# Performance work log

Measured on AMD Instinct MI355X. Metric: run time of the kernel, lower is better.

The kernel has to match this reference:

```python
import jax, jax.numpy as jnp
import numpy as np

B, S, H, D = 2, 4096, 16, 64


def setup_inputs() -> dict:
    key = jax.random.key(0)
    qkv = jax.random.normal(key, (B, S, 3, H, D), dtype=jnp.float32)
    return {"qkv": qkv}


def reference(qkv) -> jnp.ndarray:
    batch, seq_len, three, num_heads, head_dim = qkv.shape
    softmax_scale = head_dim ** (-0.5)
    q = qkv[:, :, 0]  # (B, S, H, D)
    k = qkv[:, :, 1]
    v = qkv[:, :, 2]
    # (B, H, S, S) score matrix, faithful to the naive matmul+mask+softmax path
    scores = jnp.einsum('bshd,bthd->bhst', q, k) * softmax_scale
    row = jnp.arange(seq_len)[:, None]
    col = jnp.arange(seq_len)[None, :]
    causal = row >= col  # (S, S) bool
    scores = jnp.where(causal[None, None, :, :], scores, -1000000000.0)
    attn = jax.nn.softmax(scores, axis=-1)
    out = jnp.einsum('bhst,bthd->bshd', attn, v)  # (B, S, H, D)
    return out
```

## Files before the change

kernel.cpp:

```cpp
#include <hip/hip_runtime.h>


#define S_LEN 4096
#define NHEAD 16
#define HDIM 64
#define QBLK 128
#define KVBLK 64
#define NQT (S_LEN / QBLK)
#define LDK 72
#define ROWSTRIDE (3 * NHEAD * HDIM)

using bf16x8 = __attribute__((ext_vector_type(8))) short;
using bf16x4 = __attribute__((ext_vector_type(4))) short;
using f32x4  = __attribute__((ext_vector_type(4))) float;

#define MFMA32(A, B, C) __builtin_amdgcn_mfma_f32_16x16x32_bf16((A), (B), (C), 0, 0, 0)
#define MFMA16(A, B, C) __builtin_amdgcn_mfma_f32_16x16x16bf16_1k((A), (B), (C), 0, 0, 0)

#if __has_builtin(__builtin_amdgcn_exp2f)
#define EXP2F(x) __builtin_amdgcn_exp2f(x)
#else
#define EXP2F(x) exp2f(x)
#endif

__device__ __forceinline__ int f2bf2(float lo, float hi) {
  int r;
  asm("v_cvt_pk_bf16_f32 %0, %1, %2" : "=v"(r) : "v"(lo), "v"(hi));
  return r;
}

__device__ __forceinline__ float max3f(float a, float b, float c) {
  float d;
  asm("v_max3_f32 %0, %1, %2, %3" : "=v"(d) : "v"(a), "v"(b), "v"(c));
  return d;
}

__global__ __launch_bounds__(256, 2)
void attn_fwd(const float* __restrict__ qkv, float* __restrict__ out) {
  __shared__ short Ks[KVBLK][LDK] __attribute__((aligned(16)));
  __shared__ short VTs[HDIM][LDK] __attribute__((aligned(16)));

  const int flat = (int)blockIdx.x + 32 * (int)blockIdx.y;
  const int u    = flat & 255;
  const int j    = flat >> 8;
  const int bh   = u >> 3;
  const int t8   = u & 7;
  const int qt   = (j == 0) ? t8 : (j == 1) ? 31 - t8 : (j == 2) ? 8 + t8 : 23 - t8;

  const int b    = bh >> 4;
  const int h    = bh & 15;
  const int tid  = threadIdx.x;
  const int wid  = tid >> 6;
  const int lane = tid & 63;
  const int lq   = lane & 15;
  const int lg   = lane >> 4;

  const float* basep = qkv + (size_t)b * S_LEN * ROWSTRIDE + h * HDIM;
  const float* kbase = basep + NHEAD * HDIM;
  const float* vbase = basep + 2 * NHEAD * HDIM;

  const int rb = (tid >> 4) * 4;
  const int cb = (tid & 15) * 4;
  const int vcol = 4 * ((rb >> 2) ^ (cb >> 3));

  f32x4 kreg[4], vreg[4];
  auto load_tile = [&](int kvt) {
    const int kr = kvt * KVBLK + rb;
#pragma unroll
    for (int i = 0; i < 4; ++i) {
      kreg[i] = *reinterpret_cast<const f32x4*>(kbase + (size_t)(kr + i) * ROWSTRIDE + cb);
      vreg[i] = *reinterpret_cast<const f32x4*>(vbase + (size_t)(kr + i) * ROWSTRIDE + cb);
    }
  };
  auto store_tile = [&]() {
#pragma unroll
    for (int i = 0; i < 4; ++i) {
      union { bf16x4 v; int w[2]; } kk;
      kk.w[0] = f2bf2(kreg[i][0], kreg[i][1]);
      kk.w[1] = f2bf2(kreg[i][2], kreg[i][3]);
      *reinterpret_cast<bf16x4*>(&Ks[rb + i][cb]) = kk.v;
    }
#pragma unroll
    for (int e = 0; e < 4; ++e) {
      union { bf16x4 v; int w[2]; } vv;
      vv.w[0] = f2bf2(vreg[0][e], vreg[1][e]);
      vv.w[1] = f2bf2(vreg[2][e], vreg[3][e]);
      *reinterpret_cast<bf16x4*>(&VTs[cb + e][vcol]) = vv.v;
    }
  };

  const float SC = 0.18033688011112042f;

  const int wq = qt * QBLK + wid * 32;

  bf16x8 qf[2][2];
#pragma unroll
  for (int rt = 0; rt < 2; ++rt) {
    const float* qp = basep + (size_t)(wq + rt * 16 + lq) * ROWSTRIDE + 8 * lg;
#pragma unroll
    for (int t = 0; t < 2; ++t) {
      f32x4 x0 = *reinterpret_cast<const f32x4*>(qp + 32 * t);
      f32x4 x1 = *reinterpret_cast<const f32x4*>(qp + 32 * t + 4);
      union { bf16x8 v; int w[4]; } uq;
      uq.w[0] = f2bf2(x0[0] * SC, x0[1] * SC);
      uq.w[1] = f2bf2(x0[2] * SC, x0[3] * SC);
      uq.w[2] = f2bf2(x1[0] * SC, x1[1] * SC);
      uq.w[3] = f2bf2(x1[2] * SC, x1[3] * SC);
      qf[rt][t] = uq.v;
    }
  }

  f32x4 acc[2][4];
#pragma unroll
  for (int rt = 0; rt < 2; ++rt)
#pragma unroll
    for (int dt = 0; dt < 4; ++dt)
      acc[rt][dt] = (f32x4){0.f, 0.f, 0.f, 0.f};

  float mrun[2] = {-1e30f, -1e30f};
  float lrun[2] = {0.f, 0.f};

  const int nkv = 2 * qt + 2;
  load_tile(0);

  for (int kvt = 0; kvt < nkv; ++kvt) {
    __syncthreads();
    store_tile();
    __syncthreads();
    if (kvt + 1 < nkv) load_tile(kvt + 1);

    const int kvb = kvt * KVBLK;
    if (kvb > wq + 31) continue;

    f32x4 sc[2][4];
#pragma unroll
    for (int rt = 0; rt < 2; ++rt)
#pragma unroll
      for (int c = 0; c < 4; ++c)
        sc[rt][c] = (f32x4){0.f, 0.f, 0.f, 0.f};

#pragma unroll
    for (int c = 0; c < 4; ++c) {
      bf16x8 k0 = *reinterpret_cast<const bf16x8*>(&Ks[c * 16 + lq][8 * lg]);
      bf16x8 k1 = *reinterpret_cast<const bf16x8*>(&Ks[c * 16 + lq][8 * lg + 32]);
#pragma unroll
      for (int rt = 0; rt < 2; ++rt) {
        sc[rt][c] = MFMA32(k0, qf[rt][0], sc[rt][c]);
        sc[rt][c] = MFMA32(k1, qf[rt][1], sc[rt][c]);
      }
    }

    if (kvb + KVBLK - 1 > wq) {
#pragma unroll
      for (int rt = 0; rt < 2; ++rt) {
        const int q0 = wq + rt * 16 + lq;
#pragma unroll
        for (int c = 0; c < 4; ++c)
#pragma unroll
          for (int r = 0; r < 4; ++r)
            if (kvb + c * 16 + 4 * lg + r > q0) sc[rt][c][r] = -1e30f;
      }
    }

    bf16x4 pf[2][4];
    float alpha[2];
#pragma unroll
    for (int rt = 0; rt < 2; ++rt) {
      float v0 = max3f(sc[rt][0][0], sc[rt][0][1], sc[rt][0][2]);
      float v1 = max3f(sc[rt][0][3], sc[rt][1][0], sc[rt][1][1]);
      float v2 = max3f(sc[rt][1][2], sc[rt][1][3], sc[rt][2][0]);
      float v3 = max3f(sc[rt][2][1], sc[rt][2][2], sc[rt][2][3]);
      float v4 = max3f(sc[rt][3][0], sc[rt][3][1], sc[rt][3][2]);
      float tm = fmaxf(max3f(v0, v1, v2), max3f(v3, v4, sc[rt][3][3]));
      tm = fmaxf(tm, __shfl_xor(tm, 16));
      tm = fmaxf(tm, __shfl_xor(tm, 32));
      const float newm = fmaxf(mrun[rt], tm);
      alpha[rt] = EXP2F(mrun[rt] - newm);
      mrun[rt] = newm;

      float ts = 0.f;
#pragma unroll
      for (int c = 0; c < 4; ++c) {
        float p0 = EXP2F(sc[rt][c][0] - newm);
        float p1 = EXP2F(sc[rt][c][1] - newm);
        float p2 = EXP2F(sc[rt][c][2] - newm);
        float p3 = EXP2F(sc[rt][c][3] - newm);
        ts += (p0 + p1) + (p2 + p3);
        union { bf16x4 v; int w[2]; } pp;
        pp.w[0] = f2bf2(p0, p1);
        pp.w[1] = f2bf2(p2, p3);
        pf[rt][c] = pp.v;
      }
      ts += __shfl_xor(ts, 16);
      ts += __shfl_xor(ts, 32);
      lrun[rt] = lrun[rt] * alpha[rt] + ts;
    }

#pragma unroll
    for (int rt = 0; rt < 2; ++rt) {
      const float a0 = __shfl(alpha[rt], 4 * lg + 0);
      const float a1 = __shfl(alpha[rt], 4 * lg + 1);
      const float a2 = __shfl(alpha[rt], 4 * lg + 2);
      const float a3 = __shfl(alpha[rt], 4 * lg + 3);
#pragma unroll
      for (int dt = 0; dt < 4; ++dt) {
        acc[rt][dt][0] *= a0;
        acc[rt][dt][1] *= a1;
        acc[rt][dt][2] *= a2;
        acc[rt][dt][3] *= a3;
      }
    }

#pragma unroll
    for (int dt = 0; dt < 4; ++dt) {
      const int f = (2 * dt + (lq >> 3)) & 7;
#pragma unroll
      for (int c = 0; c < 4; ++c) {
        bf16x4 vf = *reinterpret_cast<const bf16x4*>(&VTs[dt * 16 + lq][4 * ((4 * c + lg) ^ f)]);
        acc[0][dt] = MFMA16(pf[0][c], vf, acc[0][dt]);
        acc[1][dt] = MFMA16(pf[1][c], vf, acc[1][dt]);
      }
    }
  }

#pragma unroll
  for (int rt = 0; rt < 2; ++rt) {
    const float l0 = __shfl(lrun[rt], 4 * lg + 0);
    const float l1 = __shfl(lrun[rt], 4 * lg + 1);
    const float l2 = __shfl(lrun[rt], 4 * lg + 2);
    const float l3 = __shfl(lrun[rt], 4 * lg + 3);
    const f32x4 linv = {1.f / l0, 1.f / l1, 1.f / l2, 1.f / l3};
#pragma unroll
    for (int dt = 0; dt < 4; ++dt) {
#pragma unroll
      for (int r = 0; r < 4; ++r) {
        out[(size_t)(b * S_LEN + wq + rt * 16 + 4 * lg + r) * (NHEAD * HDIM) + h * HDIM + dt * 16 + lq] =
            acc[rt][dt][r] * linv[r];
      }
    }
  }
}

extern "C" void kernel_launch(void* const* d_in, const int* in_sizes, int n_in,
                              void* d_out, int out_size, void* d_ws, size_t ws_size,
                              hipStream_t stream) {
  const float* qkv = (const float*)d_in[0];
  float* o = (float*)d_out;
  dim3 grid(NQT, 2 * NHEAD);
  attn_fwd<<<grid, 256, 0, stream>>>(qkv, o);
}
```

Measured before the change: 182.4 us.

## Use 256-row Q blocks with 8 waves and paired causal tiles per block

The Q block grows to 256 rows with 512 threads (8 waves), so each K/V tile staged in LDS serves twice as many query rows. Each block now handles two query tiles, qt and 15-qt, one after the other, which evens out causal work across blocks. Staging is split so half the threads load and convert K and the other half load V. The risk is that 512 blocks of 512 threads may fill the 256 CUs less well than before, and that waves which skip fully masked tiles sit idle at the barriers.

```diff
diff --git a/kernel.cpp b/kernel.cpp
--- a/kernel.cpp
+++ b/kernel.cpp
@@ -4,9 +4,9 @@
 #define S_LEN 4096
 #define NHEAD 16
 #define HDIM 64
-#define QBLK 128
+#define QBLK 256
 #define KVBLK 64
-#define NQT (S_LEN / QBLK)
+#define NPAIR 16
 #define LDK 72
 #define ROWSTRIDE (3 * NHEAD * HDIM)
 
@@ -35,18 +35,13 @@
   return d;
 }
 
-__global__ __launch_bounds__(256, 2)
+__global__ __launch_bounds__(512, 2)
 void attn_fwd(const float* __restrict__ qkv, float* __restrict__ out) {
   __shared__ short Ks[KVBLK][LDK] __attribute__((aligned(16)));
   __shared__ short VTs[HDIM][LDK] __attribute__((aligned(16)));
 
-  const int flat = (int)blockIdx.x + 32 * (int)blockIdx.y;
-  const int u    = flat & 255;
-  const int j    = flat >> 8;
-  const int bh   = u >> 3;
-  const int t8   = u & 7;
-  const int qt   = (j == 0) ? t8 : (j == 1) ? 31 - t8 : (j == 2) ? 8 + t8 : 23 - t8;
-
+  const int qp0  = blockIdx.x;
+  const int bh   = blockIdx.y;
   const int b    = bh >> 4;
   const int h    = bh & 15;
   const int tid  = threadIdx.x;
@@ -59,183 +54,200 @@
   const float* kbase = basep + NHEAD * HDIM;
   const float* vbase = basep + 2 * NHEAD * HDIM;
 
-  const int rb = (tid >> 4) * 4;
-  const int cb = (tid & 15) * 4;
-  const int vcol = 4 * ((rb >> 2) ^ (cb >> 3));
-
-  f32x4 kreg[4], vreg[4];
+  const bool isK = tid < 256;
+  const int st   = tid & 255;
+  const int krow = st >> 2;
+  const int kcol = (st & 3) * 16;
+  const int vrb  = (st >> 4) * 4;
+  const int vcb  = (st & 15) * 4;
+  const int vcol = 4 * ((vrb >> 2) ^ (vcb >> 3));
+
+  f32x4 sreg[4];
   auto load_tile = [&](int kvt) {
-    const int kr = kvt * KVBLK + rb;
-#pragma unroll
-    for (int i = 0; i < 4; ++i) {
-      kreg[i] = *reinterpret_cast<const f32x4*>(kbase + (size_t)(kr + i) * ROWSTRIDE + cb);
-      vreg[i] = *reinterpret_cast<const f32x4*>(vbase + (size_t)(kr + i) * ROWSTRIDE + cb);
+    if (isK) {
+      const float* p = kbase + (size_t)(kvt * KVBLK + krow) * ROWSTRIDE + kcol;
+      sreg[0] = *reinterpret_cast<const f32x4*>(p);
+      sreg[1] = *reinterpret_cast<const f32x4*>(p + 4);
+      sreg[2] = *reinterpret_cast<const f32x4*>(p + 8);
+      sreg[3] = *reinterpret_cast<const f32x4*>(p + 12);
+    } else {
+      const float* p = vbase + (size_t)(kvt * KVBLK + vrb) * ROWSTRIDE + vcb;
+#pragma unroll
+      for (int i = 0; i < 4; ++i)
+        sreg[i] = *reinterpret_cast<const f32x4*>(p + (size_t)i * ROWSTRIDE);
     }
   };
   auto store_tile = [&]() {
-#pragma unroll
-    for (int i = 0; i < 4; ++i) {
-      union { bf16x4 v; int w[2]; } kk;
-      kk.w[0] = f2bf2(kreg[i][0], kreg[i][1]);
-      kk.w[1] = f2bf2(kreg[i][2], kreg[i][3]);
-      *reinterpret_cast<bf16x4*>(&Ks[rb + i][cb]) = kk.v;
-    }
-#pragma unroll
-    for (int e = 0; e < 4; ++e) {
-      union { bf16x4 v; int w[2]; } vv;
-      vv.w[0] = f2bf2(vreg[0][e], vreg[1][e]);
-      vv.w[1] = f2bf2(vreg[2][e], vreg[3][e]);
-      *reinterpret_cast<bf16x4*>(&VTs[cb + e][vcol]) = vv.v;
+    if (isK) {
+      union { bf16x8 v; int w[4]; } u0, u1;
+      u0.w[0] = f2bf2(sreg[0][0], sreg[0][1]); u0.w[1] = f2bf2(sreg[0][2], sreg[0][3]);
+      u0.w[2] = f2bf2(sreg[1][0], sreg[1][1]); u0.w[3] = f2bf2(sreg[1][2], sreg[1][3]);
+      u1.w[0] = f2bf2(sreg[2][0], sreg[2][1]); u1.w[1] = f2bf2(sreg[2][2], sreg[2][3]);
+      u1.w[2] = f2bf2(sreg[3][0], sreg[3][1]); u1.w[3] = f2bf2(sreg[3][2], sreg[3][3]);
+      *reinterpret_cast<bf16x8*>(&Ks[krow][kcol])     = u0.v;
+      *reinterpret_cast<bf16x8*>(&Ks[krow][kcol + 8]) = u1.v;
+    } else {
+#pragma unroll
+      for (int e = 0; e < 4; ++e) {
+        union { bf16x4 v; int w[2]; } vv;
+        vv.w[0] = f2bf2(sreg[0][e], sreg[1][e]);
+        vv.w[1] = f2bf2(sreg[2][e], sreg[3][e]);
+        *reinterpret_cast<bf16x4*>(&VTs[vcb + e][vcol]) = vv.v;
+      }
     }
   };
 
   const float SC = 0.18033688011112042f;
 
-  const int wq = qt * QBLK + wid * 32;
-
-  bf16x8 qf[2][2];
-#pragma unroll
-  for (int rt = 0; rt < 2; ++rt) {
-    const float* qp = basep + (size_t)(wq + rt * 16 + lq) * ROWSTRIDE + 8 * lg;
-#pragma unroll
-    for (int t = 0; t < 2; ++t) {
-      f32x4 x0 = *reinterpret_cast<const f32x4*>(qp + 32 * t);
-      f32x4 x1 = *reinterpret_cast<const f32x4*>(qp + 32 * t + 4);
-      union { bf16x8 v; int w[4]; } uq;
-      uq.w[0] = f2bf2(x0[0] * SC, x0[1] * SC);
-      uq.w[1] = f2bf2(x0[2] * SC, x0[3] * SC);
-      uq.w[2] = f2bf2(x1[0] * SC, x1[1] * SC);
-      uq.w[3] = f2bf2(x1[2] * SC, x1[3] * SC);
-      qf[rt][t] = uq.v;
-    }
-  }
-
-  f32x4 acc[2][4];
-#pragma unroll
-  for (int rt = 0; rt < 2; ++rt)
-#pragma unroll
-    for (int dt = 0; dt < 4; ++dt)
-      acc[rt][dt] = (f32x4){0.f, 0.f, 0.f, 0.f};
-
-  float mrun[2] = {-1e30f, -1e30f};
-  float lrun[2] = {0.f, 0.f};
-
-  const int nkv = 2 * qt + 2;
-  load_tile(0);
-
-  for (int kvt = 0; kvt < nkv; ++kvt) {
-    __syncthreads();
-    store_tile();
-    __syncthreads();
-    if (kvt + 1 < nkv) load_tile(kvt + 1);
-
-    const int kvb = kvt * KVBLK;
-    if (kvb > wq + 31) continue;
-
-    f32x4 sc[2][4];
+#pragma unroll 1
+  for (int pi = 0; pi < 2; ++pi) {
+    const int qt = (pi == 0) ? qp0 : (NPAIR - 1 - qp0);
+    const int wq = qt * QBLK + wid * 32;
+
+    bf16x8 qf[2][2];
+#pragma unroll
+    for (int rt = 0; rt < 2; ++rt) {
+      const float* qp = basep + (size_t)(wq + rt * 16 + lq) * ROWSTRIDE + 8 * lg;
+#pragma unroll
+      for (int t = 0; t < 2; ++t) {
+        f32x4 x0 = *reinterpret_cast<const f32x4*>(qp + 32 * t);
+        f32x4 x1 = *reinterpret_cast<const f32x4*>(qp + 32 * t + 4);
+        union { bf16x8 v; int w[4]; } uq;
+        uq.w[0] = f2bf2(x0[0] * SC, x0[1] * SC);
+        uq.w[1] = f2bf2(x0[2] * SC, x0[3] * SC);
+        uq.w[2] = f2bf2(x1[0] * SC, x1[1] * SC);
+        uq.w[3] = f2bf2(x1[2] * SC, x1[3] * SC);
+        qf[rt][t] = uq.v;
+      }
+    }
+
+    f32x4 acc[2][4];
 #pragma unroll
     for (int rt = 0; rt < 2; ++rt)
 #pragma unroll
-      for (int c = 0; c < 4; ++c)
-        sc[rt][c] = (f32x4){0.f, 0.f, 0.f, 0.f};
-
-#pragma unroll
-    for (int c = 0; c < 4; ++c) {
-      bf16x8 k0 = *reinterpret_cast<const bf16x8*>(&Ks[c * 16 + lq][8 * lg]);
-      bf16x8 k1 = *reinterpret_cast<const bf16x8*>(&Ks[c * 16 + lq][8 * lg + 32]);
+      for (int dt = 0; dt < 4; ++dt)
+        acc[rt][dt] = (f32x4){0.f, 0.f, 0.f, 0.f};
+
+    float mrun[2] = {-1e30f, -1e30f};
+    float lrun[2] = {0.f, 0.f};
+
+    const int nkv = 4 * qt + 4;
+    load_tile(0);
+
+    for (int kvt = 0; kvt < nkv; ++kvt) {
+      __syncthreads();
+      store_tile();
+      __syncthreads();
+      if (kvt + 1 < nkv) load_tile(kvt + 1);
+
+      const int kvb = kvt * KVBLK;
+      if (kvb > wq + 31) continue;
+
+      f32x4 sc[2][4];
+#pragma unroll
+      for (int rt = 0; rt < 2; ++rt)
+#pragma unroll
+        for (int c = 0; c < 4; ++c)
+          sc[rt][c] = (f32x4){0.f, 0.f, 0.f, 0.f};
+
+#pragma unroll
+      for (int c = 0; c < 4; ++c) {
+        bf16x8 k0 = *reinterpret_cast<const bf16x8*>(&Ks[c * 16 + lq][8 * lg]);
+        bf16x8 k1 = *reinterpret_cast<const bf16x8*>(&Ks[c * 16 + lq][8 * lg + 32]);
+#pragma unroll
+        for (int rt = 0; rt < 2; ++rt) {
+          sc[rt][c] = MFMA32(k0, qf[rt][0], sc[rt][c]);
+          sc[rt][c] = MFMA32(k1, qf[rt][1], sc[rt][c]);
+        }
+      }
+
+      if (kvb + KVBLK - 1 > wq) {
+#pragma unroll
+        for (int rt = 0; rt < 2; ++rt) {
+          const int q0 = wq + rt * 16 + lq;
+#pragma unroll
+          for (int c = 0; c < 4; ++c)
+#pragma unroll
+            for (int r = 0; r < 4; ++r)
+              if (kvb + c * 16 + 4 * lg + r > q0) sc[rt][c][r] = -1e30f;
+        }
+      }
+
+      bf16x4 pf[2][4];
+      float alpha[2];
 #pragma unroll
       for (int rt = 0; rt < 2; ++rt) {
-        sc[rt][c] = MFMA32(k0, qf[rt][0], sc[rt][c]);
-        sc[rt][c] = MFMA32(k1, qf[rt][1], sc[rt][c]);
-      }
-    }
-
-    if (kvb + KVBLK - 1 > wq) {
+        float v0 = max3f(sc[rt][0][0], sc[rt][0][1], sc[rt][0][2]);
+        float v1 = max3f(sc[rt][0][3], sc[rt][1][0], sc[rt][1][1]);
+        float v2 = max3f(sc[rt][1][2], sc[rt][1][3], sc[rt][2][0]);
+        float v3 = max3f(sc[rt][2][1], sc[rt][2][2], sc[rt][2][3]);
+        float v4 = max3f(sc[rt][3][0], sc[rt][3][1], sc[rt][3][2]);
+        float tm = fmaxf(max3f(v0, v1, v2), max3f(v3, v4, sc[rt][3][3]));
+        tm = fmaxf(tm, __shfl_xor(tm, 16));
+        tm = fmaxf(tm, __shfl_xor(tm, 32));
+        const float newm = fmaxf(mrun[rt], tm);
+        alpha[rt] = EXP2F(mrun[rt] - newm);
+        mrun[rt] = newm;
+
+        float ts = 0.f;
+#pragma unroll
+        for (int c = 0; c < 4; ++c) {
+          float p0 = EXP2F(sc[rt][c][0] - newm);
+          float p1 = EXP2F(sc[rt][c][1] - newm);
+          float p2 = EXP2F(sc[rt][c][2] - newm);
+          float p3 = EXP2F(sc[rt][c][3] - newm);
+          ts += (p0 + p1) + (p2 + p3);
+          union { bf16x4 v; int w[2]; } pp;
+          pp.w[0] = f2bf2(p0, p1);
+          pp.w[1] = f2bf2(p2, p3);
+          pf[rt][c] = pp.v;
+        }
+        ts += __shfl_xor(ts, 16);
+        ts += __shfl_xor(ts, 32);
+        lrun[rt] = lrun[rt] * alpha[rt] + ts;
+      }
+
 #pragma unroll
       for (int rt = 0; rt < 2; ++rt) {
-        const int q0 = wq + rt * 16 + lq;
-#pragma unroll
-        for (int c = 0; c < 4; ++c)
-#pragma unroll
-          for (int r = 0; r < 4; ++r)
-            if (kvb + c * 16 + 4 * lg + r > q0) sc[rt][c][r] = -1e30f;
-      }
-    }
-
-    bf16x4 pf[2][4];
-    float alpha[2];
+        const float a0 = __shfl(alpha[rt], 4 * lg + 0);
+        const float a1 = __shfl(alpha[rt], 4 * lg + 1);
+        const float a2 = __shfl(alpha[rt], 4 * lg + 2);
+        const float a3 = __shfl(alpha[rt], 4 * lg + 3);
+#pragma unroll
+        for (int dt = 0; dt < 4; ++dt) {
+          acc[rt][dt][0] *= a0;
+          acc[rt][dt][1] *= a1;
+          acc[rt][dt][2] *= a2;
+          acc[rt][dt][3] *= a3;
+        }
+      }
+
+#pragma unroll
+      for (int dt = 0; dt < 4; ++dt) {
+        const int f = (2 * dt + (lq >> 3)) & 7;
+#pragma unroll
+        for (int c = 0; c < 4; ++c) {
+          bf16x4 vf = *reinterpret_cast<const bf16x4*>(&VTs[dt * 16 + lq][4 * ((4 * c + lg) ^ f)]);
+          acc[0][dt] = MFMA16(pf[0][c], vf, acc[0][dt]);
+          acc[1][dt] = MFMA16(pf[1][c], vf, acc[1][dt]);
+        }
+      }
+    }
+
 #pragma unroll
     for (int rt = 0; rt < 2; ++rt) {
-      float v0 = max3f(sc[rt][0][0], sc[rt][0][1], sc[rt][0][2]);
-      float v1 = max3f(sc[rt][0][3], sc[rt][1][0], sc[rt][1][1]);
-      float v2 = max3f(sc[rt][1][2], sc[rt][1][3], sc[rt][2][0]);
-      float v3 = max3f(sc[rt][2][1], sc[rt][2][2], sc[rt][2][3]);
-      float v4 = max3f(sc[rt][3][0], sc[rt][3][1], sc[rt][3][2]);
-      float tm = fmaxf(max3f(v0, v1, v2), max3f(v3, v4, sc[rt][3][3]));
-      tm = fmaxf(tm, __shfl_xor(tm, 16));
-      tm = fmaxf(tm, __shfl_xor(tm, 32));
-      const float newm = fmaxf(mrun[rt], tm);
-      alpha[rt] = EXP2F(mrun[rt] - newm);
-      mrun[rt] = newm;
-
-      float ts = 0.f;
-#pragma unroll
-      for (int c = 0; c < 4; ++c) {
-        float p0 = EXP2F(sc[rt][c][0] - newm);
-        float p1 = EXP2F(sc[rt][c][1] - newm);
-        float p2 = EXP2F(sc[rt][c][2] - newm);
-        float p3 = EXP2F(sc[rt][c][3] - newm);
-        ts += (p0 + p1) + (p2 + p3);
-        union { bf16x4 v; int w[2]; } pp;
-        pp.w[0] = f2bf2(p0, p1);
-        pp.w[1] = f2bf2(p2, p3);
-        pf[rt][c] = pp.v;
-      }
-      ts += __shfl_xor(ts, 16);
-      ts += __shfl_xor(ts, 32);
-      lrun[rt] = lrun[rt] * alpha[rt] + ts;
-    }
-
-#pragma unroll
-    for (int rt = 0; rt < 2; ++rt) {
-      const float a0 = __shfl(alpha[rt], 4 * lg + 0);
-      const float a1 = __shfl(alpha[rt], 4 * lg + 1);
-      const float a2 = __shfl(alpha[rt], 4 * lg + 2);
-      const float a3 = __shfl(alpha[rt], 4 * lg + 3);
+      const float l0 = __shfl(lrun[rt], 4 * lg + 0);
+      const float l1 = __shfl(lrun[rt], 4 * lg + 1);
+      const float l2 = __shfl(lrun[rt], 4 * lg + 2);
+      const float l3 = __shfl(lrun[rt], 4 * lg + 3);
+      const f32x4 linv = {1.f / l0, 1.f / l1, 1.f / l2, 1.f / l3};
 #pragma unroll
       for (int dt = 0; dt < 4; ++dt) {
-        acc[rt][dt][0] *= a0;
-        acc[rt][dt][1] *= a1;
-        acc[rt][dt][2] *= a2;
-        acc[rt][dt][3] *= a3;
-      }
-    }
-
-#pragma unroll
-    for (int dt = 0; dt < 4; ++dt) {
-      const int f = (2 * dt + (lq >> 3)) & 7;
-#pragma unroll
-      for (int c = 0; c < 4; ++c) {
-        bf16x4 vf = *reinterpret_cast<const bf16x4*>(&VTs[dt * 16 + lq][4 * ((4 * c + lg) ^ f)]);
-        acc[0][dt] = MFMA16(pf[0][c], vf, acc[0][dt]);
-        acc[1][dt] = MFMA16(pf[1][c], vf, acc[1][dt]);
-      }
-    }
-  }
-
-#pragma unroll
-  for (int rt = 0; rt < 2; ++rt) {
-    const float l0 = __shfl(lrun[rt], 4 * lg + 0);
-    const float l1 = __shfl(lrun[rt], 4 * lg + 1);
-    const float l2 = __shfl(lrun[rt], 4 * lg + 2);
-    const float l3 = __shfl(lrun[rt], 4 * lg + 3);
-    const f32x4 linv = {1.f / l0, 1.f / l1, 1.f / l2, 1.f / l3};
-#pragma unroll
-    for (int dt = 0; dt < 4; ++dt) {
-#pragma unroll
-      for (int r = 0; r < 4; ++r) {
-        out[(size_t)(b * S_LEN + wq + rt * 16 + 4 * lg + r) * (NHEAD * HDIM) + h * HDIM + dt * 16 + lq] =
-            acc[rt][dt][r] * linv[r];
+#pragma unroll
+        for (int r = 0; r < 4; ++r) {
+          out[(size_t)(b * S_LEN + wq + rt * 16 + 4 * lg + r) * (NHEAD * HDIM) + h * HDIM + dt * 16 + lq] =
+              acc[rt][dt][r] * linv[r];
+        }
       }
     }
   }
@@ -246,6 +258,6 @@
                               hipStream_t stream) {
   const float* qkv = (const float*)d_in[0];
   float* o = (float*)d_out;
-  dim3 grid(NQT, 2 * NHEAD);
-  attn_fwd<<<grid, 256, 0, stream>>>(qkv, o);
-}
+  dim3 grid(NPAIR, 2 * NHEAD);
+  attn_fwd<<<grid, 512, 0, stream>>>(qkv, o);
+}
```

Measured after the change: 262.2 us. 43.8% more time.

## Precompute bf16 K and transposed V into workspace, read directly from global

Applied to the files above, without the earlier changes.

Adds a pre-pass kernel that converts K to bf16 and writes V transposed in bf16 into the workspace buffer. The attention kernel then loads its MFMA fragments straight from global or L2, with no LDS staging and no __syncthreads. Each wave also stops at its own causal bound instead of looping over the whole block's tile count. This removes repeated fp32 conversion, the barriers, and LDS traffic, at the cost of an extra launch and uncoalesced small global loads that are not double-buffered. The old path is kept as a fallback for when the workspace is too small.

```diff
diff --git a/kernel.cpp b/kernel.cpp
--- a/kernel.cpp
+++ b/kernel.cpp
@@ -9,6 +9,7 @@
 #define NQT (S_LEN / QBLK)
 #define LDK 72
 #define ROWSTRIDE (3 * NHEAD * HDIM)
+#define KB_ELEMS ((size_t)2 * NHEAD * S_LEN * HDIM)
 
 using bf16x8 = __attribute__((ext_vector_type(8))) short;
 using bf16x4 = __attribute__((ext_vector_type(4))) short;
@@ -36,10 +37,56 @@
 }
 
 __global__ __launch_bounds__(256, 2)
-void attn_fwd(const float* __restrict__ qkv, float* __restrict__ out) {
-  __shared__ short Ks[KVBLK][LDK] __attribute__((aligned(16)));
-  __shared__ short VTs[HDIM][LDK] __attribute__((aligned(16)));
-
+void precompute_kv(const float* __restrict__ qkv, short* __restrict__ Kb,
+                   short* __restrict__ VTb) {
+  const int s0 = blockIdx.x * 64;
+  const int bh = blockIdx.y;
+  const int b  = bh >> 4;
+  const int h  = bh & 15;
+  const int tid = threadIdx.x;
+  const float* basep = qkv + (size_t)b * S_LEN * ROWSTRIDE + h * HDIM;
+  const float* kbase = basep + NHEAD * HDIM;
+  const float* vbase = basep + 2 * NHEAD * HDIM;
+
+  {
+    const int krow = tid >> 2;
+    const int kcol = (tid & 3) * 16;
+    const float* p = kbase + (size_t)(s0 + krow) * ROWSTRIDE + kcol;
+    f32x4 a0 = *reinterpret_cast<const f32x4*>(p);
+    f32x4 a1 = *reinterpret_cast<const f32x4*>(p + 4);
+    f32x4 a2 = *reinterpret_cast<const f32x4*>(p + 8);
+    f32x4 a3 = *reinterpret_cast<const f32x4*>(p + 12);
+    union { bf16x8 v; int w[4]; } u0, u1;
+    u0.w[0] = f2bf2(a0[0], a0[1]); u0.w[1] = f2bf2(a0[2], a0[3]);
+    u0.w[2] = f2bf2(a1[0], a1[1]); u0.w[3] = f2bf2(a1[2], a1[3]);
+    u1.w[0] = f2bf2(a2[0], a2[1]); u1.w[1] = f2bf2(a2[2], a2[3]);
+    u1.w[2] = f2bf2(a3[0], a3[1]); u1.w[3] = f2bf2(a3[2], a3[3]);
+    short* dst = Kb + ((size_t)bh * S_LEN + s0 + krow) * HDIM + kcol;
+    *reinterpret_cast<bf16x8*>(dst)     = u0.v;
+    *reinterpret_cast<bf16x8*>(dst + 8) = u1.v;
+  }
+  {
+    const int vrb = (tid >> 4) * 4;
+    const int vcb = (tid & 15) * 4;
+    const float* p = vbase + (size_t)(s0 + vrb) * ROWSTRIDE + vcb;
+    f32x4 r0 = *reinterpret_cast<const f32x4*>(p);
+    f32x4 r1 = *reinterpret_cast<const f32x4*>(p + ROWSTRIDE);
+    f32x4 r2 = *reinterpret_cast<const f32x4*>(p + 2 * ROWSTRIDE);
+    f32x4 r3 = *reinterpret_cast<const f32x4*>(p + 3 * ROWSTRIDE);
+#pragma unroll
+    for (int e = 0; e < 4; ++e) {
+      union { bf16x4 v; int w[2]; } vv;
+      vv.w[0] = f2bf2(r0[e], r1[e]);
+      vv.w[1] = f2bf2(r2[e], r3[e]);
+      short* dst = VTb + ((size_t)bh * HDIM + vcb + e) * S_LEN + s0 + vrb;
+      *reinterpret_cast<bf16x4*>(dst) = vv.v;
+    }
+  }
+}
+
+__global__ __launch_bounds__(256, 2)
+void attn_fwd(const float* __restrict__ qkv, const short* __restrict__ Kb,
+              const short* __restrict__ VTb, float* __restrict__ out) {
   const int flat = (int)blockIdx.x + 32 * (int)blockIdx.y;
   const int u    = flat & 255;
   const int j    = flat >> 8;
@@ -56,39 +103,6 @@
   const int lg   = lane >> 4;
 
   const float* basep = qkv + (size_t)b * S_LEN * ROWSTRIDE + h * HDIM;
-  const float* kbase = basep + NHEAD * HDIM;
-  const float* vbase = basep + 2 * NHEAD * HDIM;
-
-  const int rb = (tid >> 4) * 4;
-  const int cb = (tid & 15) * 4;
-  const int vcol = 4 * ((rb >> 2) ^ (cb >> 3));
-
-  f32x4 kreg[4], vreg[4];
-  auto load_tile = [&](int kvt) {
-    const int kr = kvt * KVBLK + rb;
-#pragma unroll
-    for (int i = 0; i < 4; ++i) {
-      kreg[i] = *reinterpret_cast<const f32x4*>(kbase + (size_t)(kr + i) * ROWSTRIDE + cb);
-      vreg[i] = *reinterpret_cast<const f32x4*>(vbase + (size_t)(kr + i) * ROWSTRIDE + cb);
-    }
-  };
-  auto store_tile = [&]() {
-#pragma unroll
-    for (int i = 0; i < 4; ++i) {
-      union { bf16x4 v; int w[2]; } kk;
-      kk.w[0] = f2bf2(kreg[i][0], kreg[i][1]);
-      kk.w[1] = f2bf2(kreg[i][2], kreg[i][3]);
-      *reinterpret_cast<bf16x4*>(&Ks[rb + i][cb]) = kk.v;
-    }
-#pragma unroll
-    for (int e = 0; e < 4; ++e) {
-      union { bf16x4 v; int w[2]; } vv;
-      vv.w[0] = f2bf2(vreg[0][e], vreg[1][e]);
-      vv.w[1] = f2bf2(vreg[2][e], vreg[3][e]);
-      *reinterpret_cast<bf16x4*>(&VTs[cb + e][vcol]) = vv.v;
-    }
-  };
-
   const float SC = 0.18033688011112042f;
 
   const int wq = qt * QBLK + wid * 32;
@@ -120,17 +134,14 @@
   float mrun[2] = {-1e30f, -1e30f};
   float lrun[2] = {0.f, 0.f};
 
-  const int nkv = 2 * qt + 2;
-  load_tile(0);
-
+  const int nkv = ((wq + 31) >> 6) + 1;
+
+  const short* kwave = Kb + ((size_t)bh * S_LEN + lq) * HDIM + 8 * lg;
+  const short* vwave = VTb + ((size_t)bh * HDIM + lq) * S_LEN + 4 * lg;
+
+#pragma unroll 1
   for (int kvt = 0; kvt < nkv; ++kvt) {
-    __syncthreads();
-    store_tile();
-    __syncthreads();
-    if (kvt + 1 < nkv) load_tile(kvt + 1);
-
     const int kvb = kvt * KVBLK;
-    if (kvb > wq + 31) continue;
 
     f32x4 sc[2][4];
 #pragma unroll
@@ -141,8 +152,9 @@
 
 #pragma unroll
     for (int c = 0; c < 4; ++c) {
-      bf16x8 k0 = *reinterpret_cast<const bf16x8*>(&Ks[c * 16 + lq][8 * lg]);
-      bf16x8 k1 = *reinterpret_cast<const bf16x8*>(&Ks[c * 16 + lq][8 * lg + 32]);
+      const short* kp = kwave + (size_t)(kvb + c * 16) * HDIM;
+      bf16x8 k0 = *reinterpret_cast<const bf16x8*>(kp);
+      bf16x8 k1 = *reinterpret_cast<const bf16x8*>(kp + 32);
 #pragma unroll
       for (int rt = 0; rt < 2; ++rt) {
         sc[rt][c] = MFMA32(k0, qf[rt][0], sc[rt][c]);
@@ -213,10 +225,10 @@
 
 #pragma unroll
     for (int dt = 0; dt < 4; ++dt) {
-      const int f = (2 * dt + (lq >> 3)) & 7;
+      const short* vp = vwave + (size_t)(dt * 16) * S_LEN + kvb;
 #pragma unroll
       for (int c = 0; c < 4; ++c) {
-        bf16x4 vf = *reinterpret_cast<const bf16x4*>(&VTs[dt * 16 + lq][4 * ((4 * c + lg) ^ f)]);
+        bf16x4 vf = *reinterpret_cast<const bf16x4*>(vp + c * 16);
         acc[0][dt] = MFMA16(pf[0][c], vf, acc[0][dt]);
         acc[1][dt] = MFMA16(pf[1][c], vf, acc[1][dt]);
       }
@@ -241,11 +253,222 @@
   }
 }
 
+__global__ __launch_bounds__(256, 2)
+void attn_fwd_fb(const float* __restrict__ qkv, float* __restrict__ out) {
+  __shared__ short Ks[KVBLK][LDK] __attribute__((aligned(16)));
+  __shared__ short VTs[HDIM][LDK] __attribute__((aligned(16)));
+
+  const int flat = (int)blockIdx.x + 32 * (int)blockIdx.y;
+  const int u    = flat & 255;
+  const int j    = flat >> 8;
+  const int bh   = u >> 3;
+  const int t8   = u & 7;
+  const int qt   = (j == 0) ? t8 : (j == 1) ? 31 - t8 : (j == 2) ? 8 + t8 : 23 - t8;
+
+  const int b    = bh >> 4;
+  const int h    = bh & 15;
+  const int tid  = threadIdx.x;
+  const int wid  = tid >> 6;
+  const int lane = tid & 63;
+  const int lq   = lane & 15;
+  const int lg   = lane >> 4;
+
+  const float* basep = qkv + (size_t)b * S_LEN * ROWSTRIDE + h * HDIM;
+  const float* kbase = basep + NHEAD * HDIM;
+  const float* vbase = basep + 2 * NHEAD * HDIM;
+
+  const int rb = (tid >> 4) * 4;
+  const int cb = (tid & 15) * 4;
+  const int vcol = 4 * ((rb >> 2) ^ (cb >> 3));
+
+  f32x4 kreg[4], vreg[4];
+  auto load_tile = [&](int kvt) {
+    const int kr = kvt * KVBLK + rb;
+#pragma unroll
+    for (int i = 0; i < 4; ++i) {
+      kreg[i] = *reinterpret_cast<const f32x4*>(kbase + (size_t)(kr + i) * ROWSTRIDE + cb);
+      vreg[i] = *reinterpret_cast<const f32x4*>(vbase + (size_t)(kr + i) * ROWSTRIDE + cb);
+    }
+  };
+  auto store_tile = [&]() {
+#pragma unroll
+    for (int i = 0; i < 4; ++i) {
+      union { bf16x4 v; int w[2]; } kk;
+      kk.w[0] = f2bf2(kreg[i][0], kreg[i][1]);
+      kk.w[1] = f2bf2(kreg[i][2], kreg[i][3]);
+      *reinterpret_cast<bf16x4*>(&Ks[rb + i][cb]) = kk.v;
+    }
+#pragma unroll
+    for (int e = 0; e < 4; ++e) {
+      union { bf16x4 v; int w[2]; } vv;
+      vv.w[0] = f2bf2(vreg[0][e], vreg[1][e]);
+      vv.w[1] = f2bf2(vreg[2][e], vreg[3][e]);
+      *reinterpret_cast<bf16x4*>(&VTs[cb + e][vcol]) = vv.v;
+    }
+  };
+
+  const float SC = 0.18033688011112042f;
+  const int wq = qt * QBLK + wid * 32;
+
+  bf16x8 qf[2][2];
+#pragma unroll
+  for (int rt = 0; rt < 2; ++rt) {
+    const float* qp = basep + (size_t)(wq + rt * 16 + lq) * ROWSTRIDE + 8 * lg;
+#pragma unroll
+    for (int t = 0; t < 2; ++t) {
+      f32x4 x0 = *reinterpret_cast<const f32x4*>(qp + 32 * t);
+      f32x4 x1 = *reinterpret_cast<const f32x4*>(qp + 32 * t + 4);
+      union { bf16x8 v; int w[4]; } uq;
+      uq.w[0] = f2bf2(x0[0] * SC, x0[1] * SC);
+      uq.w[1] = f2bf2(x0[2] * SC, x0[3] * SC);
+      uq.w[2] = f2bf2(x1[0] * SC, x1[1] * SC);
+      uq.w[3] = f2bf2(x1[2] * SC, x1[3] * SC);
+      qf[rt][t] = uq.v;
+    }
+  }
+
+  f32x4 acc[2][4];
+#pragma unroll
+  for (int rt = 0; rt < 2; ++rt)
+#pragma unroll
+    for (int dt = 0; dt < 4; ++dt)
+      acc[rt][dt] = (f32x4){0.f, 0.f, 0.f, 0.f};
+
+  float mrun[2] = {-1e30f, -1e30f};
+  float lrun[2] = {0.f, 0.f};
+
+  const int nkv = 2 * qt + 2;
+  load_tile(0);
+
+  for (int kvt = 0; kvt < nkv; ++kvt) {
+    __syncthreads();
+    store_tile();
+    __syncthreads();
+    if (kvt + 1 < nkv) load_tile(kvt + 1);
+
+    const int kvb = kvt * KVBLK;
+    if (kvb > wq + 31) continue;
+
+    f32x4 sc[2][4];
+#pragma unroll
+    for (int rt = 0; rt < 2; ++rt)
+#pragma unroll
+      for (int c = 0; c < 4; ++c)
+        sc[rt][c] = (f32x4){0.f, 0.f, 0.f, 0.f};
+
+#pragma unroll
+    for (int c = 0; c < 4; ++c) {
+      bf16x8 k0 = *reinterpret_cast<const bf16x8*>(&Ks[c * 16 + lq][8 * lg]);
+      bf16x8 k1 = *reinterpret_cast<const bf16x8*>(&Ks[c * 16 + lq][8 * lg + 32]);
+#pragma unroll
+      for (int rt = 0; rt < 2; ++rt) {
+        sc[rt][c] = MFMA32(k0, qf[rt][0], sc[rt][c]);
+        sc[rt][c] = MFMA32(k1, qf[rt][1], sc[rt][c]);
+      }
+    }
+
+    if (kvb + KVBLK - 1 > wq) {
+#pragma unroll
+      for (int rt = 0; rt < 2; ++rt) {
+        const int q0 = wq + rt * 16 + lq;
+#pragma unroll
+        for (int c = 0; c < 4; ++c)
+#pragma unroll
+          for (int r = 0; r < 4; ++r)
+            if (kvb + c * 16 + 4 * lg + r > q0) sc[rt][c][r] = -1e30f;
+      }
+    }
+
+    bf16x4 pf[2][4];
+    float alpha[2];
+#pragma unroll
+    for (int rt = 0; rt < 2; ++rt) {
+      float v0 = max3f(sc[rt][0][0], sc[rt][0][1], sc[rt][0][2]);
+      float v1 = max3f(sc[rt][0][3], sc[rt][1][0], sc[rt][1][1]);
+      float v2 = max3f(sc[rt][1][2], sc[rt][1][3], sc[rt][2][0]);
+      float v3 = max3f(sc[rt][2][1], sc[rt][2][2], sc[rt][2][3]);
+      float v4 = max3f(sc[rt][3][0], sc[rt][3][1], sc[rt][3][2]);
+      float tm = fmaxf(max3f(v0, v1, v2), max3f(v3, v4, sc[rt][3][3]));
+      tm = fmaxf(tm, __shfl_xor(tm, 16));
+      tm = fmaxf(tm, __shfl_xor(tm, 32));
+      const float newm = fmaxf(mrun[rt], tm);
+      alpha[rt] = EXP2F(mrun[rt] - newm);
+      mrun[rt] = newm;
+
+      float ts = 0.f;
+#pragma unroll
+      for (int c = 0; c < 4; ++c) {
+        float p0 = EXP2F(sc[rt][c][0] - newm);
+        float p1 = EXP2F(sc[rt][c][1] - newm);
+        float p2 = EXP2F(sc[rt][c][2] - newm);
+        float p3 = EXP2F(sc[rt][c][3] - newm);
+        ts += (p0 + p1) + (p2 + p3);
+        union { bf16x4 v; int w[2]; } pp;
+        pp.w[0] = f2bf2(p0, p1);
+        pp.w[1] = f2bf2(p2, p3);
+        pf[rt][c] = pp.v;
+      }
+      ts += __shfl_xor(ts, 16);
+      ts += __shfl_xor(ts, 32);
+      lrun[rt] = lrun[rt] * alpha[rt] + ts;
+    }
+
+#pragma unroll
+    for (int rt = 0; rt < 2; ++rt) {
+      const float a0 = __shfl(alpha[rt], 4 * lg + 0);
+      const float a1 = __shfl(alpha[rt], 4 * lg + 1);
+      const float a2 = __shfl(alpha[rt], 4 * lg + 2);
+      const float a3 = __shfl(alpha[rt], 4 * lg + 3);
+#pragma unroll
+      for (int dt = 0; dt < 4; ++dt) {
+        acc[rt][dt][0] *= a0;
+        acc[rt][dt][1] *= a1;
+        acc[rt][dt][2] *= a2;
+        acc[rt][dt][3] *= a3;
+      }
+    }
+
+#pragma unroll
+    for (int dt = 0; dt < 4; ++dt) {
+      const int f = (2 * dt + (lq >> 3)) & 7;
+#pragma unroll
+      for (int c = 0; c < 4; ++c) {
+        bf16x4 vf = *reinterpret_cast<const bf16x4*>(&VTs[dt * 16 + lq][4 * ((4 * c + lg) ^ f)]);
+        acc[0][dt] = MFMA16(pf[0][c], vf, acc[0][dt]);
+        acc[1][dt] = MFMA16(pf[1][c], vf, acc[1][dt]);
+      }
+    }
+  }
+
+#pragma unroll
+  for (int rt = 0; rt < 2; ++rt) {
+    const float l0 = __shfl(lrun[rt], 4 * lg + 0);
+    const float l1 = __shfl(lrun[rt], 4 * lg + 1);
+    const float l2 = __shfl(lrun[rt], 4 * lg + 2);
+    const float l3 = __shfl(lrun[rt], 4 * lg + 3);
+    const f32x4 linv = {1.f / l0, 1.f / l1, 1.f / l2, 1.f / l3};
+#pragma unroll
+    for (int dt = 0; dt < 4; ++dt) {
+#pragma unroll
+      for (int r = 0; r < 4; ++r) {
+        out[(size_t)(b * S_LEN + wq + rt * 16 + 4 * lg + r) * (NHEAD * HDIM) + h * HDIM + dt * 16 + lq] =
+            acc[rt][dt][r] * linv[r];
+      }
+    }
+  }
+}
+
 extern "C" void kernel_launch(void* const* d_in, const int* in_sizes, int n_in,
                               void* d_out, int out_size, void* d_ws, size_t ws_size,
                               hipStream_t stream) {
   const float* qkv = (const float*)d_in[0];
   float* o = (float*)d_out;
-  dim3 grid(NQT, 2 * NHEAD);
-  attn_fwd<<<grid, 256, 0, stream>>>(qkv, o);
-}
+  if (ws_size >= 2 * KB_ELEMS * sizeof(short)) {
+    short* Kb  = (short*)d_ws;
+    short* VTb = Kb + KB_ELEMS;
+    precompute_kv<<<dim3(S_LEN / 64, 2 * NHEAD), 256, 0, stream>>>(qkv, Kb, VTb);
+    attn_fwd<<<dim3(32, 32), 256, 0, stream>>>(qkv, Kb, VTb, o);
+  } else {
+    attn_fwd_fb<<<dim3(32, 32), 256, 0, stream>>>(qkv, o);
+  }
+}
```

Measured after the change: 417.8 us. +129.0%, slower.

## Double the query tile to 256 rows with four row tiles per wave

Applied to the files above, without the earlier changes.

Raises the query block from 128 to 256 rows so each wave processes 64 query rows (four 16-row MFMA tiles) against every staged K/V tile. This halves the global K/V loads and bf16 conversions per query row. The grid remapping now pairs light and heavy causal tiles two at a time, and the alpha rescale is folded into the per-row-tile softmax loop. In exchange it raises register pressure for the accumulators, scores and Q fragments, halves the number of blocks to 512, and increases the masked waste on diagonal tiles, all of which can hurt occupancy and load balance.

```diff
diff --git a/kernel.cpp b/kernel.cpp
--- a/kernel.cpp
+++ b/kernel.cpp
@@ -4,9 +4,10 @@
 #define S_LEN 4096
 #define NHEAD 16
 #define HDIM 64
-#define QBLK 128
+#define QBLK 256
 #define KVBLK 64
 #define NQT (S_LEN / QBLK)
+#define RT 4
 #define LDK 72
 #define ROWSTRIDE (3 * NHEAD * HDIM)
 
@@ -40,12 +41,12 @@
   __shared__ short Ks[KVBLK][LDK] __attribute__((aligned(16)));
   __shared__ short VTs[HDIM][LDK] __attribute__((aligned(16)));
 
-  const int flat = (int)blockIdx.x + 32 * (int)blockIdx.y;
+  const int flat = (int)blockIdx.x + 16 * (int)blockIdx.y;
   const int u    = flat & 255;
   const int j    = flat >> 8;
   const int bh   = u >> 3;
   const int t8   = u & 7;
-  const int qt   = (j == 0) ? t8 : (j == 1) ? 31 - t8 : (j == 2) ? 8 + t8 : 23 - t8;
+  const int qt   = j ? (NQT - 1 - t8) : t8;
 
   const int b    = bh >> 4;
   const int h    = bh & 15;
@@ -91,11 +92,11 @@
 
   const float SC = 0.18033688011112042f;
 
-  const int wq = qt * QBLK + wid * 32;
-
-  bf16x8 qf[2][2];
-#pragma unroll
-  for (int rt = 0; rt < 2; ++rt) {
+  const int wq = qt * QBLK + wid * 64;
+
+  bf16x8 qf[RT][2];
+#pragma unroll
+  for (int rt = 0; rt < RT; ++rt) {
     const float* qp = basep + (size_t)(wq + rt * 16 + lq) * ROWSTRIDE + 8 * lg;
 #pragma unroll
     for (int t = 0; t < 2; ++t) {
@@ -110,19 +111,20 @@
     }
   }
 
-  f32x4 acc[2][4];
-#pragma unroll
-  for (int rt = 0; rt < 2; ++rt)
+  f32x4 acc[RT][4];
+#pragma unroll
+  for (int rt = 0; rt < RT; ++rt)
 #pragma unroll
     for (int dt = 0; dt < 4; ++dt)
       acc[rt][dt] = (f32x4){0.f, 0.f, 0.f, 0.f};
 
-  float mrun[2] = {-1e30f, -1e30f};
-  float lrun[2] = {0.f, 0.f};
-
-  const int nkv = 2 * qt + 2;
+  float mrun[RT] = {-1e30f, -1e30f, -1e30f, -1e30f};
+  float lrun[RT] = {0.f, 0.f, 0.f, 0.f};
+
+  const int nkv = 4 * qt + 4;
   load_tile(0);
 
+#pragma unroll 1
   for (int kvt = 0; kvt < nkv; ++kvt) {
     __syncthreads();
     store_tile();
@@ -130,11 +132,11 @@
     if (kvt + 1 < nkv) load_tile(kvt + 1);
 
     const int kvb = kvt * KVBLK;
-    if (kvb > wq + 31) continue;
-
-    f32x4 sc[2][4];
-#pragma unroll
-    for (int rt = 0; rt < 2; ++rt)
+    if (kvb > wq + 63) continue;
+
+    f32x4 sc[RT][4];
+#pragma unroll
+    for (int rt = 0; rt < RT; ++rt)
 #pragma unroll
       for (int c = 0; c < 4; ++c)
         sc[rt][c] = (f32x4){0.f, 0.f, 0.f, 0.f};
@@ -144,7 +146,7 @@
       bf16x8 k0 = *reinterpret_cast<const bf16x8*>(&Ks[c * 16 + lq][8 * lg]);
       bf16x8 k1 = *reinterpret_cast<const bf16x8*>(&Ks[c * 16 + lq][8 * lg + 32]);
 #pragma unroll
-      for (int rt = 0; rt < 2; ++rt) {
+      for (int rt = 0; rt < RT; ++rt) {
         sc[rt][c] = MFMA32(k0, qf[rt][0], sc[rt][c]);
         sc[rt][c] = MFMA32(k1, qf[rt][1], sc[rt][c]);
       }
@@ -152,7 +154,7 @@
 
     if (kvb + KVBLK - 1 > wq) {
 #pragma unroll
-      for (int rt = 0; rt < 2; ++rt) {
+      for (int rt = 0; rt < RT; ++rt) {
         const int q0 = wq + rt * 16 + lq;
 #pragma unroll
         for (int c = 0; c < 4; ++c)
@@ -162,10 +164,9 @@
       }
     }
 
-    bf16x4 pf[2][4];
-    float alpha[2];
-#pragma unroll
-    for (int rt = 0; rt < 2; ++rt) {
+    bf16x4 pf[RT][4];
+#pragma unroll
+    for (int rt = 0; rt < RT; ++rt) {
       float v0 = max3f(sc[rt][0][0], sc[rt][0][1], sc[rt][0][2]);
       float v1 = max3f(sc[rt][0][3], sc[rt][1][0], sc[rt][1][1]);
       float v2 = max3f(sc[rt][1][2], sc[rt][1][3], sc[rt][2][0]);
@@ -175,7 +176,7 @@
       tm = fmaxf(tm, __shfl_xor(tm, 16));
       tm = fmaxf(tm, __shfl_xor(tm, 32));
       const float newm = fmaxf(mrun[rt], tm);
-      alpha[rt] = EXP2F(mrun[rt] - newm);
+      const float alpha = EXP2F(mrun[rt] - newm);
       mrun[rt] = newm;
 
       float ts = 0.f;
@@ -193,15 +194,12 @@
       }
       ts += __shfl_xor(ts, 16);
       ts += __shfl_xor(ts, 32);
-      lrun[rt] = lrun[rt] * alpha[rt] + ts;
-    }
-
-#pragma unroll
-    for (int rt = 0; rt < 2; ++rt) {
-      const float a0 = __shfl(alpha[rt], 4 * lg + 0);
-      const float a1 = __shfl(alpha[rt], 4 * lg + 1);
-      const float a2 = __shfl(alpha[rt], 4 * lg + 2);
-      const float a3 = __shfl(alpha[rt], 4 * lg + 3);
+      lrun[rt] = lrun[rt] * alpha + ts;
+
+      const float a0 = __shfl(alpha, 4 * lg + 0);
+      const float a1 = __shfl(alpha, 4 * lg + 1);
+      const float a2 = __shfl(alpha, 4 * lg + 2);
+      const float a3 = __shfl(alpha, 4 * lg + 3);
 #pragma unroll
       for (int dt = 0; dt < 4; ++dt) {
         acc[rt][dt][0] *= a0;
@@ -217,14 +215,15 @@
 #pragma unroll
       for (int c = 0; c < 4; ++c) {
         bf16x4 vf = *reinterpret_cast<const bf16x4*>(&VTs[dt * 16 + lq][4 * ((4 * c + lg) ^ f)]);
-        acc[0][dt] = MFMA16(pf[0][c], vf, acc[0][dt]);
-        acc[1][dt] = MFMA16(pf[1][c], vf, acc[1][dt]);
+#pragma unroll
+        for (int rt = 0; rt < RT; ++rt)
+          acc[rt][dt] = MFMA16(pf[rt][c], vf, acc[rt][dt]);
       }
     }
   }
 
 #pragma unroll
-  for (int rt = 0; rt < 2; ++rt) {
+  for (int rt = 0; rt < RT; ++rt) {
     const float l0 = __shfl(lrun[rt], 4 * lg + 0);
     const float l1 = __shfl(lrun[rt], 4 * lg + 1);
     const float l2 = __shfl(lrun[rt], 4 * lg + 2);
```

New measurement: 239.9 us. 31.5% more time.
